# Kernel tuning notes

Hardware: AMD Instinct MI355X
Metric: run time of the kernel (lower is better)

Reference implementation:

```python
import jax, jax.numpy as jnp
import numpy as np

EPS = 1e-5
NEG_SLOPE = 0.2
B, C, P, K, E, H = 16, 16, 2048, 16, 64, 2


def cross_set_gather(f, idx):
    # f: (B, C, P), idx: (B, P, K) -> (B, C, P, K)
    return jax.vmap(lambda fb, ib: fb[:, ib])(f, idx)


def bn(x, g, b, m, v, axes):
    # x normalized along channel dim; g,b,m,v shaped to broadcast via `axes` reshape
    return (x - m.reshape(axes)) * (g.reshape(axes) / jnp.sqrt(v.reshape(axes) + EPS)) + b.reshape(axes)


def setup_inputs() -> dict:
    key = jax.random.key(0)
    ks = jax.random.split(key, 16)
    features = jax.random.normal(ks[0], (B, C, P), dtype=jnp.float32)
    neighbor_indices = jax.random.randint(ks[1], (B, P, K), 0, P)
    mask = jax.random.randint(ks[2], (B, 1, P), 0, 2).astype(bool)
    s = 0.1
    return {
        "features": features,
        "neighbor_indices": neighbor_indices,
        "mask": mask,
        "node_w": jax.random.normal(ks[3], (H, E, C)) * s,
        "node_g": jnp.ones((H, E)),
        "node_b": jnp.zeros((H, E)),
        "node_m": jax.random.normal(ks[4], (H, E)) * s,
        "node_v": jax.random.uniform(ks[5], (H, E)) + 0.5,
        "edge_w": jax.random.normal(ks[6], (H, E, C)) * s,
        "edge_bias": jax.random.normal(ks[7], (H, E)) * s,
        "edge_g": jnp.ones((H, E)),
        "edge_b2": jnp.zeros((H, E)),
        "edge_m": jax.random.normal(ks[8], (H, E)) * s,
        "edge_v": jax.random.uniform(ks[9], (H, E)) + 0.5,
        "self_w": jax.random.normal(ks[10], (H, E)) * s,
        "self_b": jax.random.normal(ks[11], (H,)) * s,
        "nb_w": jax.random.normal(ks[12], (H, E)) * s,
        "nb_b": jax.random.normal(ks[13], (H,)) * s,
    }


def _forward(features, neighbor_indices, mask, node_w, node_g, node_b, node_m, node_v,
             edge_w, edge_bias, edge_g, edge_b2, edge_m, edge_v, self_w, self_b, nb_w, nb_b):
    mask_f = mask.astype(features.dtype)  # (B,1,P)
    # node encoding (Conv1d k=1 + BN): (B,H,E,P)
    nodes = jnp.einsum('hec,bcp->bhep', node_w, features)
    nodes = bn(nodes, node_g, node_b, node_m, node_v, (1, H, E, 1))
    # edge features: neighbor - center, (B,C,P,K)
    nbr = cross_set_gather(features, neighbor_indices)
    edge_feat = nbr - features[:, :, :, None]
    # edge encoding (Conv2d k=1 + BN): (B,H,E,P,K)
    enc = jnp.einsum('hec,bcpk->bhepk', edge_w, edge_feat) + edge_bias[None, :, :, None, None]
    enc = bn(enc, edge_g, edge_b2, edge_m, edge_v, (1, H, E, 1, 1))
    # attention scores
    self_score = jnp.einsum('he,bhep->bhp', self_w, nodes) + self_b[None, :, None]  # (B,H,P)
    nb_score = jnp.einsum('he,bhepk->bhpk', nb_w, enc) + nb_b[None, :, None, None]  # (B,H,P,K)
    logits = self_score[..., None] + nb_score
    logits = jnp.where(logits >= 0, logits, NEG_SLOPE * logits)  # leaky_relu(0.2)
    # neighbor validity mask: (B,P,K)
    valid = cross_set_gather(mask_f, neighbor_indices)[:, 0]
    vb = valid[:, None, :, :]  # (B,1,P,K)
    logits = jnp.where(vb == 0, -jnp.inf, logits)
    coef = jnp.nan_to_num(jax.nn.softmax(logits, axis=-1), nan=0.0, posinf=0.0, neginf=0.0)  # (B,H,P,K)
    # weighted aggregation + relu: (B,H,E,P)
    att = jax.nn.relu(jnp.einsum('bhpk,bhepk->bhep', coef, enc))
    # graph features: masked max over K
    enc_masked = jnp.where(vb[:, :, None, :, :] == 0, -jnp.inf, enc)
    graph = jnp.max(enc_masked, axis=-1)  # (B,H,E,P)
    graph = jnp.where(jnp.isinf(graph), 0.0, graph)
    # multi-head combine: element-wise max over heads, then mask
    att_out = jnp.max(att, axis=1) * mask_f  # (B,E,P)
    graph_out = jnp.max(graph, axis=1) * mask_f  # (B,E,P)
    return att_out, graph_out


def reference(features, neighbor_indices, mask, node_w, node_g, node_b, node_m, node_v,
              edge_w, edge_bias, edge_g, edge_b2, edge_m, edge_v, self_w, self_b, nb_w, nb_b):
    return _forward(features, neighbor_indices, mask, node_w, node_g, node_b, node_m, node_v,
                    edge_w, edge_bias, edge_g, edge_b2, edge_m, edge_v, self_w, self_b, nb_w, nb_b)
```

## Files before the change

kernel.cpp:

```cpp
#include <hip/hip_runtime.h>
#include <hip/hip_bf16.h>
#include <hip/hip_fp16.h>
#include <math.h>

#define NB 16
#define NC 16
#define NP 2048
#define NK 16
#define NE 64
#define NH 2
#define EPSV 1e-5f
#define NSLOPE 0.2f
#define QINV -1e30f
#define QTHR -1e29f

#define WS_SECB  12288
#define WS_CNB2  13312
#define WS_PINFO 16384
#define WS_EPB   2162688

__device__ __forceinline__ float ldf(const void* p, int i, int isb) {
  return isb ? __bfloat162float(((const __hip_bfloat16*)p)[i]) : ((const float*)p)[i];
}
__device__ __forceinline__ unsigned f2bf(float f) {
  unsigned u = __float_as_uint(f);
  return (u + 0x7FFFu + ((u >> 16) & 1u)) >> 16;
}
__device__ __forceinline__ float bflo(unsigned v) { return __uint_as_float(v << 16); }
__device__ __forceinline__ float bfhi(unsigned v) { return __uint_as_float(v & 0xFFFF0000u); }

__global__ void __launch_bounds__(256) k_proj(
    const void* feat, const void* mask,
    const void* edge_w, const void* node_w,
    const void* edge_g, const void* edge_v, const void* edge_bias,
    const void* edge_m, const void* edge_b2,
    const void* node_g, const void* node_v, const void* node_b, const void* node_m,
    const void* self_w, const void* self_b, const void* nb_w, const void* nb_b,
    char* ws)
{
  __shared__ int sh_isb, sh_mbyte;
  __shared__ float ewl[128*17];
  __shared__ float nwl[128*17];
  __shared__ float fl[NC][64];
  __shared__ float w2[128], wn[128], ctr[128];
  __shared__ float s_wq[32], s_wsc[32], s_cself[2];

  const int tid = threadIdx.x;
  const int w = tid >> 6, lane = tid & 63;

  if (w == 0) {
    const unsigned short* u = (const unsigned short*)feat;
    int cnt = 0;
#pragma unroll
    for (int i = 0; i < 8; i++) {
      int ex = (u[lane*8 + i] >> 7) & 0xFF;
      cnt += (ex >= 100 && ex <= 135) ? 1 : 0;
    }
#pragma unroll
    for (int o = 32; o >= 1; o >>= 1) cnt += __shfl_xor(cnt, o);
    if (lane == 0) sh_isb = (cnt >= 460) ? 1 : 0;
  }
  if (w == 1) {
    const unsigned char* mb = (const unsigned char*)mask;
    int c = 0;
#pragma unroll
    for (int i = 0; i < 16; i++) {
      int ix = lane*16 + i;
      c += ((ix & 3) && mb[ix]) ? 1 : 0;
    }
#pragma unroll
    for (int o = 32; o >= 1; o >>= 1) c += __shfl_xor(c, o);
    if (lane == 0) sh_mbyte = (c > 0) ? 1 : 0;
  }
  __syncthreads();
  const int isb = sh_isb, mbyte = sh_mbyte;

  const int bid = blockIdx.x;
  const int b  = (bid & 7)*2 + ((bid >> 3) & 1);
  const int pt = bid >> 4;
  const int p0 = pt * 64;

  for (int i = tid; i < 128*16; i += 256) {
    const int he = i >> 4, c = i & 15;
    ewl[he*17 + c] = ldf(edge_w, i, isb);
    nwl[he*17 + c] = ldf(node_w, i, isb);
  }
  for (int i = tid; i < NC*64; i += 256) {
    int c = i >> 6, p = i & 63;
    fl[c][p] = ldf(feat, (b*NC + c)*NP + p0 + p, isb);
  }
  if (tid < 128) {
    const int he = tid, h = tid >> 6;
    float se = ldf(edge_g, he, isb) * rsqrtf(ldf(edge_v, he, isb) + EPSV);
    float cb = se * (ldf(edge_bias, he, isb) - ldf(edge_m, he, isb)) + ldf(edge_b2, he, isb);
    float ns = ldf(node_g, he, isb) * rsqrtf(ldf(node_v, he, isb) + EPSV);
    w2[he]  = ldf(nb_w, he, isb) * se;
    wn[he]  = ldf(self_w, he, isb) * ns;
    ctr[he] = ldf(self_w, he, isb) * (ldf(node_b, he, isb) - ldf(node_m, he, isb) * ns);
    if (bid == 0) {
      ((float2*)(ws + WS_SECB))[he] = make_float2(se, cb);
      float t = ldf(nb_w, he, isb) * cb;
#pragma unroll
      for (int o = 32; o >= 1; o >>= 1) t += __shfl_xor(t, o);
      if ((tid & 63) == 0)
        ((float*)(ws + WS_CNB2))[h] = t + ldf(nb_b, h, isb);
    }
  }
  if (bid == 0 && tid == 0) {
    ((int*)ws)[0] = isb;
    ((int*)ws)[1] = mbyte;
  }
  __syncthreads();
  if (tid < 32) {
    const int h = tid >> 4, c = tid & 15;
    float sq = 0.f, sn = 0.f;
#pragma unroll 8
    for (int e = 0; e < NE; e++) {
      sq += w2[h*NE+e] * ewl[(h*NE+e)*17 + c];
      sn += wn[h*NE+e] * nwl[(h*NE+e)*17 + c];
    }
    s_wq[tid]  = sq;
    s_wsc[tid] = sn;
  }
  if (tid < 2) {
    float cs = 0.f;
#pragma unroll 8
    for (int e = 0; e < NE; e++) cs += ctr[tid*NE+e];
    s_cself[tid] = cs + ldf(self_b, tid, isb);
  }
  __syncthreads();

  const int e = tid & 63;
  const int pp = tid >> 6;
  float wv0[NC], wv1[NC];
#pragma unroll
  for (int c = 0; c < NC; c++) {
    wv0[c] = ewl[e*17 + c];
    wv1[c] = ewl[(NE + e)*17 + c];
  }
  unsigned* epb = (unsigned*)(ws + WS_EPB);
  const long base = (long)(b*NP + p0) * 64;
  for (int pass = 0; pass < 16; pass++) {
    const int p = pass*4 + pp;
    float a0 = 0.f, a1 = 0.f;
#pragma unroll
    for (int c = 0; c < NC; c++) {
      const float f = fl[c][p];
      a0 = fmaf(wv0[c], f, a0);
      a1 = fmaf(wv1[c], f, a1);
    }
    epb[base + (long)p*64 + e] = f2bf(a0) | (f2bf(a1) << 16);
  }

  if (tid < 64) {
    float q0=0.f, q1=0.f, s0=0.f, s1=0.f;
#pragma unroll
    for (int c = 0; c < NC; c++) {
      const float f = fl[c][tid];
      q0 = fmaf(s_wq[c],     f, q0);
      q1 = fmaf(s_wq[16+c],  f, q1);
      s0 = fmaf(s_wsc[c],    f, s0);
      s1 = fmaf(s_wsc[16+c], f, s1);
    }
    const int p = p0 + tid;
    bool mv;
    if (mbyte) mv = ((const unsigned char*)mask)[b*NP + p] != 0;
    else       mv = ((const int*)mask)[b*NP + p] != 0;
    float4 pi;
    pi.x = mv ? q0 : QINV;
    pi.y = mv ? q1 : QINV;
    pi.z = s0 + s_cself[0];
    pi.w = s1 + s_cself[1];
    ((float4*)(ws + WS_PINFO))[b*NP + p] = pi;
  }
}

__global__ void __launch_bounds__(256) k_main(const int* nidx, char* ws, void* out)
{
  __shared__ float sh_se[128], sh_cbe[128], sh_cnb[2];
  __shared__ uint2 ent[32][17];
  __shared__ unsigned char cntcm[32];
  __shared__ float att_t[NE][33];
  __shared__ float gr_t[NE][33];

  const int tid  = threadIdx.x;
  const int w    = tid >> 6;
  const int lane = tid & 63;

  const int isb = ((const int*)ws)[0];
  if (tid < 128) {
    const float2 sc = ((const float2*)(ws + WS_SECB))[tid];
    sh_se[tid]  = sc.x;
    sh_cbe[tid] = sc.y;
  }
  if (tid < 2) sh_cnb[tid] = ((const float*)(ws + WS_CNB2))[tid];
  __syncthreads();

  const float4* pinfo = (const float4*)(ws + WS_PINFO);
  const int bid = blockIdx.x;
  const int b  = (bid & 7)*2 + ((bid >> 3) & 1);
  const int pt = bid >> 4;
  const int p0 = pt * 32;
  const float cnb0 = sh_cnb[0], cnb1 = sh_cnb[1];

  {
    const int pl = w*8 + (lane >> 3);
    const int p  = p0 + pl;
    const int kk = (lane & 7) * 2;
    const float4 Pc = pinfo[b*NP + p];
    const bool cm = (Pc.x > QTHR);
    const int2 iv = *(const int2*)(nidx + ((long)b*NP + p)*NK + kk);
    const float2 Q0 = *(const float2*)&pinfo[b*NP + iv.x];
    const float2 Q1 = *(const float2*)&pinfo[b*NP + iv.y];
    const bool v0 = (Q0.x > QTHR), v1 = (Q1.x > QTHR);

    float l00 = Pc.z + Q0.x - Pc.x + cnb0;  l00 = (l00 >= 0.f) ? l00 : NSLOPE*l00;
    float l01 = Pc.w + Q0.y - Pc.y + cnb1;  l01 = (l01 >= 0.f) ? l01 : NSLOPE*l01;
    float l10 = Pc.z + Q1.x - Pc.x + cnb0;  l10 = (l10 >= 0.f) ? l10 : NSLOPE*l10;
    float l11 = Pc.w + Q1.y - Pc.y + cnb1;  l11 = (l11 >= 0.f) ? l11 : NSLOPE*l11;
    l00 = v0 ? l00 : -INFINITY;  l01 = v0 ? l01 : -INFINITY;
    l10 = v1 ? l10 : -INFINITY;  l11 = v1 ? l11 : -INFINITY;

    float mx0 = fmaxf(l00, l10), mx1 = fmaxf(l01, l11);
#pragma unroll
    for (int o = 1; o <= 4; o <<= 1) {
      mx0 = fmaxf(mx0, __shfl_xor(mx0, o));
      mx1 = fmaxf(mx1, __shfl_xor(mx1, o));
    }
    const float e00 = __expf(l00 - mx0), e10 = __expf(l10 - mx0);
    const float e01 = __expf(l01 - mx1), e11 = __expf(l11 - mx1);
    float s0 = e00 + e10, s1 = e01 + e11;
#pragma unroll
    for (int o = 1; o <= 4; o <<= 1) {
      s0 += __shfl_xor(s0, o);
      s1 += __shfl_xor(s1, o);
    }
    const float inv0 = 1.f / s0, inv1 = 1.f / s1;

    unsigned vmask = ((v0 ? 1u : 0u) << kk) | ((v1 ? 1u : 0u) << (kk + 1));
#pragma unroll
    for (int o = 1; o <= 4; o <<= 1) vmask |= __shfl_xor(vmask, o);

    const int pos0 = __popc(vmask & ((1u << kk) - 1));
    if (v0) {
      const __half2 h2 = __floats2half2_rn(e00 * inv0, e01 * inv1);
      uint2 en; en.x = *(const unsigned*)&h2; en.y = ((unsigned)iv.x) << 8;
      ent[pl][pos0] = en;
    }
    if (v1) {
      const __half2 h2 = __floats2half2_rn(e10 * inv0, e11 * inv1);
      uint2 en; en.x = *(const unsigned*)&h2; en.y = ((unsigned)iv.y) << 8;
      ent[pl][pos0 + (v0 ? 1 : 0)] = en;
    }
    if ((lane & 7) == 0)
      cntcm[pl] = (unsigned char)(__popc(vmask) | (cm ? 0x80 : 0));
  }
  __syncthreads();

  const float se0 = sh_se[lane],  se1 = sh_se[NE + lane];
  const float cb0 = sh_cbe[lane], cb1 = sh_cbe[NE + lane];
  const char* epb_b = ws + WS_EPB + (long)b * NP * 256;

  for (int j = 0; j < 8; j++) {
    const int pl = w*8 + j;
    const unsigned cc = cntcm[pl];
    if (!(cc & 0x80)) { att_t[lane][pl] = 0.f; gr_t[lane][pl] = 0.f; continue; }
    const int cnt = cc & 0x7F;

    const unsigned rawp = *(const unsigned*)(epb_b + (long)(p0 + pl)*256 + lane*4);
    const float ra0 = bflo(rawp), ra1 = bfhi(rawp);
    const float cpe0 = cb0 - se0*ra0, cpe1 = cb1 - se1*ra1;

    float a0 = 0.f, a1 = 0.f;
    float mx0 = -INFINITY, mn0 = INFINITY, mx1 = -INFINITY, mn1 = INFINITY;
#pragma unroll 4
    for (int k = 0; k < cnt; k++) {
      const uint2 en = ent[pl][k];
      const float2 cf = __half22float2(*(const __half2*)&en.x);
      const unsigned v = *(const unsigned*)(epb_b + en.y + lane*4);
      const float v0 = bflo(v), v1 = bfhi(v);
      a0 = fmaf(cf.x, v0, a0);
      a1 = fmaf(cf.y, v1, a1);
      mx0 = fmaxf(mx0, v0); mn0 = fminf(mn0, v0);
      mx1 = fmaxf(mx1, v1); mn1 = fminf(mn1, v1);
    }
    const bool av = (cnt > 0);
    const float csel = av ? 1.f : 0.f;
    const float att0 = fmaxf(fmaf(se0, a0, cpe0*csel), 0.f);
    const float att1 = fmaxf(fmaf(se1, a1, cpe1*csel), 0.f);
    const float g0 = av ? fmaf(se0, (se0 >= 0.f) ? mx0 : mn0, cpe0) : 0.f;
    const float g1 = av ? fmaf(se1, (se1 >= 0.f) ? mx1 : mn1, cpe1) : 0.f;
    att_t[lane][pl] = fmaxf(att0, att1);
    gr_t[lane][pl]  = fmaxf(g0, g1);
  }
  __syncthreads();

  const long obase = (long)b * NE * NP;
  const long go = (long)NB * NE * NP;
  for (int i = tid; i < NE*16; i += 256) {
    const int ee = i >> 4, pp = (i & 15) * 2;
    const long oi = obase + (long)ee * NP + p0 + pp;
    const float a0 = att_t[ee][pp], a1 = att_t[ee][pp+1];
    const float g0 = gr_t[ee][pp],  g1 = gr_t[ee][pp+1];
    if (isb) {
      __hip_bfloat16* o = (__hip_bfloat16*)out;
      *(ushort2*)&o[oi]      = make_ushort2((unsigned short)f2bf(a0), (unsigned short)f2bf(a1));
      *(ushort2*)&o[oi + go] = make_ushort2((unsigned short)f2bf(g0), (unsigned short)f2bf(g1));
    } else {
      float* o = (float*)out;
      *(float2*)&o[oi]      = make_float2(a0, a1);
      *(float2*)&o[oi + go] = make_float2(g0, g1);
    }
  }
}

extern "C" void kernel_launch(void* const* d_in, const int* in_sizes, int n_in,
                              void* d_out, int out_size, void* d_ws, size_t ws_size,
                              hipStream_t stream)
{
  const void* feat      = d_in[0];
  const void* nidx      = d_in[1];
  const void* mask      = d_in[2];
  const void* node_w    = d_in[3];
  const void* node_g    = d_in[4];
  const void* node_b    = d_in[5];
  const void* node_m    = d_in[6];
  const void* node_v    = d_in[7];
  const void* edge_w    = d_in[8];
  const void* edge_bias = d_in[9];
  const void* edge_g    = d_in[10];
  const void* edge_b2   = d_in[11];
  const void* edge_m    = d_in[12];
  const void* edge_v    = d_in[13];
  const void* self_w    = d_in[14];
  const void* self_b    = d_in[15];
  const void* nb_w      = d_in[16];
  const void* nb_b      = d_in[17];
  char* ws = (char*)d_ws;

  hipLaunchKernelGGL(k_proj, dim3(NB*(NP/64)), dim3(256), 0, stream,
                     feat, mask, edge_w, node_w,
                     edge_g, edge_v, edge_bias, edge_m, edge_b2,
                     node_g, node_v, node_b, node_m,
                     self_w, self_b, nb_w, nb_b, ws);
  hipLaunchKernelGGL(k_main, dim3(NB*(NP/32)), dim3(256), 0, stream,
                     (const int*)nidx, ws, d_out);
}
```

Before: 119.7 us.

## Skip edge projection for masked points and split point info into compact arrays

The mask tile is loaded into shared memory once, and the per-point edge projection store is skipped for masked-out points, whose projections are never used downstream. The float4 point-info array is split into separate q and s float2 arrays, so the neighbor gather in the main kernel reads a denser 8-byte array. The small weight-reduction dot products are spread across more threads using shuffle reductions. The risks are warp divergence in the skip loop and an extra global array.

```diff
diff --git a/kernel.cpp b/kernel.cpp
--- a/kernel.cpp
+++ b/kernel.cpp
@@ -16,7 +16,8 @@
 
 #define WS_SECB  12288
 #define WS_CNB2  13312
-#define WS_PINFO 16384
+#define WS_PQ    16384
+#define WS_PS    278528
 #define WS_EPB   2162688
 
 __device__ __forceinline__ float ldf(const void* p, int i, int isb) {
@@ -44,6 +45,7 @@
   __shared__ float fl[NC][64];
   __shared__ float w2[128], wn[128], ctr[128];
   __shared__ float s_wq[32], s_wsc[32], s_cself[2];
+  __shared__ unsigned char mtile[64];
 
   const int tid = threadIdx.x;
   const int w = tid >> 6, lane = tid & 63;
@@ -89,8 +91,14 @@
     int c = i >> 6, p = i & 63;
     fl[c][p] = ldf(feat, (b*NC + c)*NP + p0 + p, isb);
   }
-  if (tid < 128) {
-    const int he = tid, h = tid >> 6;
+  if (tid < 64) {
+    bool mv;
+    if (mbyte) mv = ((const unsigned char*)mask)[b*NP + p0 + tid] != 0;
+    else       mv = ((const int*)mask)[b*NP + p0 + tid] != 0;
+    mtile[tid] = mv ? 1 : 0;
+  }
+  if (tid >= 64 && tid < 192) {
+    const int he = tid - 64, h = he >> 6;
     float se = ldf(edge_g, he, isb) * rsqrtf(ldf(edge_v, he, isb) + EPSV);
     float cb = se * (ldf(edge_bias, he, isb) - ldf(edge_m, he, isb)) + ldf(edge_b2, he, isb);
     float ns = ldf(node_g, he, isb) * rsqrtf(ldf(node_v, he, isb) + EPSV);
@@ -102,7 +110,7 @@
       float t = ldf(nb_w, he, isb) * cb;
 #pragma unroll
       for (int o = 32; o >= 1; o >>= 1) t += __shfl_xor(t, o);
-      if ((tid & 63) == 0)
+      if ((he & 63) == 0)
         ((float*)(ws + WS_CNB2))[h] = t + ldf(nb_b, h, isb);
     }
   }
@@ -111,22 +119,27 @@
     ((int*)ws)[1] = mbyte;
   }
   __syncthreads();
-  if (tid < 32) {
-    const int h = tid >> 4, c = tid & 15;
+
+  if (tid < 128) {
+    const int h = tid >> 6, c = (tid >> 2) & 15, eq = tid & 3;
     float sq = 0.f, sn = 0.f;
-#pragma unroll 8
-    for (int e = 0; e < NE; e++) {
+#pragma unroll
+    for (int i = 0; i < 16; i++) {
+      const int e = eq*16 + i;
       sq += w2[h*NE+e] * ewl[(h*NE+e)*17 + c];
       sn += wn[h*NE+e] * nwl[(h*NE+e)*17 + c];
     }
-    s_wq[tid]  = sq;
-    s_wsc[tid] = sn;
-  }
-  if (tid < 2) {
+    sq += __shfl_xor(sq, 1); sq += __shfl_xor(sq, 2);
+    sn += __shfl_xor(sn, 1); sn += __shfl_xor(sn, 2);
+    if (eq == 0) { s_wq[h*16 + c] = sq; s_wsc[h*16 + c] = sn; }
+  }
+  if (tid >= 128 && tid < 136) {
+    const int h = (tid - 128) >> 2, eq = tid & 3;
     float cs = 0.f;
-#pragma unroll 8
-    for (int e = 0; e < NE; e++) cs += ctr[tid*NE+e];
-    s_cself[tid] = cs + ldf(self_b, tid, isb);
+#pragma unroll
+    for (int i = 0; i < 16; i++) cs += ctr[h*NE + eq*16 + i];
+    cs += __shfl_xor(cs, 1); cs += __shfl_xor(cs, 2);
+    if (eq == 0) s_cself[h] = cs + ldf(self_b, h, isb);
   }
   __syncthreads();
 
@@ -142,6 +155,7 @@
   const long base = (long)(b*NP + p0) * 64;
   for (int pass = 0; pass < 16; pass++) {
     const int p = pass*4 + pp;
+    if (!mtile[p]) continue;
     float a0 = 0.f, a1 = 0.f;
 #pragma unroll
     for (int c = 0; c < NC; c++) {
@@ -163,15 +177,9 @@
       s1 = fmaf(s_wsc[16+c], f, s1);
     }
     const int p = p0 + tid;
-    bool mv;
-    if (mbyte) mv = ((const unsigned char*)mask)[b*NP + p] != 0;
-    else       mv = ((const int*)mask)[b*NP + p] != 0;
-    float4 pi;
-    pi.x = mv ? q0 : QINV;
-    pi.y = mv ? q1 : QINV;
-    pi.z = s0 + s_cself[0];
-    pi.w = s1 + s_cself[1];
-    ((float4*)(ws + WS_PINFO))[b*NP + p] = pi;
+    const bool mv = mtile[tid] != 0;
+    ((float2*)(ws + WS_PQ))[b*NP + p] = make_float2(mv ? q0 : QINV, mv ? q1 : QINV);
+    ((float2*)(ws + WS_PS))[b*NP + p] = make_float2(s0 + s_cself[0], s1 + s_cself[1]);
   }
 }
 
@@ -196,7 +204,8 @@
   if (tid < 2) sh_cnb[tid] = ((const float*)(ws + WS_CNB2))[tid];
   __syncthreads();
 
-  const float4* pinfo = (const float4*)(ws + WS_PINFO);
+  const float2* Pq = (const float2*)(ws + WS_PQ);
+  const float2* Ps = (const float2*)(ws + WS_PS);
   const int bid = blockIdx.x;
   const int b  = (bid & 7)*2 + ((bid >> 3) & 1);
   const int pt = bid >> 4;
@@ -207,17 +216,18 @@
     const int pl = w*8 + (lane >> 3);
     const int p  = p0 + pl;
     const int kk = (lane & 7) * 2;
-    const float4 Pc = pinfo[b*NP + p];
-    const bool cm = (Pc.x > QTHR);
+    const float2 Pcq = Pq[b*NP + p];
+    const float2 Pcs = Ps[b*NP + p];
+    const bool cm = (Pcq.x > QTHR);
     const int2 iv = *(const int2*)(nidx + ((long)b*NP + p)*NK + kk);
-    const float2 Q0 = *(const float2*)&pinfo[b*NP + iv.x];
-    const float2 Q1 = *(const float2*)&pinfo[b*NP + iv.y];
+    const float2 Q0 = Pq[b*NP + iv.x];
+    const float2 Q1 = Pq[b*NP + iv.y];
     const bool v0 = (Q0.x > QTHR), v1 = (Q1.x > QTHR);
 
-    float l00 = Pc.z + Q0.x - Pc.x + cnb0;  l00 = (l00 >= 0.f) ? l00 : NSLOPE*l00;
-    float l01 = Pc.w + Q0.y - Pc.y + cnb1;  l01 = (l01 >= 0.f) ? l01 : NSLOPE*l01;
-    float l10 = Pc.z + Q1.x - Pc.x + cnb0;  l10 = (l10 >= 0.f) ? l10 : NSLOPE*l10;
-    float l11 = Pc.w + Q1.y - Pc.y + cnb1;  l11 = (l11 >= 0.f) ? l11 : NSLOPE*l11;
+    float l00 = Pcs.x + Q0.x - Pcq.x + cnb0;  l00 = (l00 >= 0.f) ? l00 : NSLOPE*l00;
+    float l01 = Pcs.y + Q0.y - Pcq.y + cnb1;  l01 = (l01 >= 0.f) ? l01 : NSLOPE*l01;
+    float l10 = Pcs.x + Q1.x - Pcq.x + cnb0;  l10 = (l10 >= 0.f) ? l10 : NSLOPE*l10;
+    float l11 = Pcs.y + Q1.y - Pcq.y + cnb1;  l11 = (l11 >= 0.f) ? l11 : NSLOPE*l11;
     l00 = v0 ? l00 : -INFINITY;  l01 = v0 ? l01 : -INFINITY;
     l10 = v1 ? l10 : -INFINITY;  l11 = v1 ? l11 : -INFINITY;
 
```

Measured after the change: 117.7 us. About the same (-1.6%).
